# Kernel optimization log

Measured on AMD Instinct MI355X. Metric: run time of the kernel, lower is better.

## Reference

```python
import jax, jax.numpy as jnp
import numpy as np

N_STATE = 1024
N_HEAD = 16
HEAD_DIM = N_STATE // N_HEAD
SCALE = HEAD_DIM ** (-0.25)


def setup_inputs() -> dict:
    key = jax.random.key(0)
    ks = jax.random.split(key, 9)
    B, S, D = 32, 1500, N_STATE
    std = 1.0 / np.sqrt(D)
    return {
        "hidden_states": jax.random.normal(ks[0], (B, 1, D), dtype=jnp.float32),
        "encoder_output": jax.random.normal(ks[1], (B, S, D), dtype=jnp.float32),
        "Wq": jax.random.normal(ks[2], (D, D), dtype=jnp.float32) * std,
        "bq": jax.random.normal(ks[3], (D,), dtype=jnp.float32) * std,
        "Wk": jax.random.normal(ks[4], (D, D), dtype=jnp.float32) * std,
        "Wv": jax.random.normal(ks[5], (D, D), dtype=jnp.float32) * std,
        "bv": jax.random.normal(ks[6], (D,), dtype=jnp.float32) * std,
        "Wo": jax.random.normal(ks[7], (D, D), dtype=jnp.float32) * std,
        "bo": jax.random.normal(ks[8], (D,), dtype=jnp.float32) * std,
    }


def reference(hidden_states, encoder_output, Wq, bq, Wk, Wv, bv, Wo, bo):
    B = hidden_states.shape[0]
    S = encoder_output.shape[1]
    # projections (torch F.linear: x @ W.T + b)
    q = hidden_states @ Wq.T + bq                  # [B, 1, D]
    k_original = encoder_output @ Wk.T             # [B, S, D] (no bias)
    v_original = encoder_output @ Wv.T + bv        # [B, S, D]

    q = q.reshape(B, 1, N_HEAD, HEAD_DIM).transpose(0, 2, 1, 3)         # [B,H,1,hd]
    k = k_original.reshape(B, S, N_HEAD, HEAD_DIM).transpose(0, 2, 1, 3)  # [B,H,S,hd]
    v = v_original.reshape(B, S, N_HEAD, HEAD_DIM).transpose(0, 2, 1, 3)  # [B,H,S,hd]

    # pre-scaled q and k, scores in fp32 softmax then cast back
    attn_weights = jnp.einsum('bhqd,bhkd->bhqk', q * SCALE, k * SCALE)  # [B,H,1,S]
    attn_weights = jax.nn.softmax(attn_weights.astype(jnp.float32), axis=-1).astype(q.dtype)
    attn_output = jnp.einsum('bhqk,bhkd->bhqd', attn_weights, v)        # [B,H,1,hd]
    attn_output = attn_output.transpose(0, 2, 1, 3).reshape(B, 1, N_STATE)
    attn_output = attn_output @ Wo.T + bo
    return attn_output, k_original, v_original
```

## Files before the change

kernel.cpp:

```cpp
#include <hip/hip_runtime.h>
#include <cstdint>
#include <cstddef>

#define D_MODEL 1024
#define NH      16
#define HD      64
#define B_SZ    32
#define SEQ     1500
#define MROWS   (B_SZ * SEQ)
#define KD      1024
#define NCH     16
#define PSTR    68

typedef __attribute__((ext_vector_type(8))) short bf16x8;
typedef __attribute__((ext_vector_type(4))) float f32x4;
typedef unsigned short u16;

__device__ __forceinline__ u16 f2b(float f) {
  unsigned int x = __float_as_uint(f);
  x = (x + 0x7FFFu + ((x >> 16) & 1u)) >> 16;
  return (u16)x;
}

#define CAST_BLOCKS 3072
#define QPROJ_BLOCKS 64

__global__ __launch_bounds__(256) void cast_all_q(const float* __restrict__ enc,
                                                  const float* __restrict__ Wk,
                                                  const float* __restrict__ Wv,
                                                  const float* __restrict__ hs,
                                                  const float* __restrict__ Wq,
                                                  const float* __restrict__ bq,
                                                  u16* __restrict__ encb,
                                                  u16* __restrict__ wkvb,
                                                  float* __restrict__ qs) {
  const int tid = threadIdx.x;
  if (blockIdx.x < CAST_BLOCKS) {
    const int NA = MROWS * KD / 8;
    const int NW = KD * KD / 8;
    int stride = CAST_BLOCKS * 256;
    for (int i = blockIdx.x * 256 + tid; i < NA + 2 * NW; i += stride) {
      const float* s; u16* d;
      if (i < NA)            { s = enc + (size_t)i * 8;            d = encb + (size_t)i * 8; }
      else if (i < NA + NW)  { size_t j = i - NA;      s = Wk + j * 8; d = wkvb + j * 8; }
      else                   { size_t j = i - NA - NW; s = Wv + j * 8; d = wkvb + (size_t)NW * 8 + j * 8; }
      const float4* s4 = reinterpret_cast<const float4*>(s);
      float4 a = s4[0], b = s4[1];
      u16 u[8];
      u[0]=f2b(a.x); u[1]=f2b(a.y); u[2]=f2b(a.z); u[3]=f2b(a.w);
      u[4]=f2b(b.x); u[5]=f2b(b.y); u[6]=f2b(b.z); u[7]=f2b(b.w);
      *reinterpret_cast<uint4*>(d) = *reinterpret_cast<const uint4*>(u);
    }
  } else {
    const int qb = blockIdx.x - CAST_BLOCKS;
    const int n  = qb * 16 + (tid & 15);
    const int bb = tid >> 4;
    const float4* wp  = (const float4*)(Wq + (size_t)n * D_MODEL);
    const float4* x0p = (const float4*)(hs + (size_t)bb * D_MODEL);
    const float4* x1p = (const float4*)(hs + (size_t)(bb + 16) * D_MODEL);
    float a0 = 0.f, a1 = 0.f;
    #pragma unroll 8
    for (int i = 0; i < D_MODEL / 4; ++i) {
      float4 w = wp[i], x0 = x0p[i], x1 = x1p[i];
      a0 += w.x * x0.x + w.y * x0.y + w.z * x0.z + w.w * x0.w;
      a1 += w.x * x1.x + w.y * x1.y + w.z * x1.z + w.w * x1.w;
    }
    const float bqn = bq[n];
    qs[(size_t)bb * D_MODEL + n]        = (a0 + bqn) * 0.125f;
    qs[(size_t)(bb + 16) * D_MODEL + n] = (a1 + bqn) * 0.125f;
  }
}

#define GBM 128
#define GBN 256
#define GBK 32
#define GNT (KD / GBK)

__device__ __forceinline__ void stageA(const u16* __restrict__ Ag, u16* lbuf,
                                       long m0, int kt, int tid) {
  int c = tid;
  int r = c >> 2, cp = c & 3;
  int scp = cp ^ ((r >> 1) & 3);
  const u16* src = Ag + (m0 + r) * (long)KD + kt * GBK + scp * 8;
  __builtin_amdgcn_global_load_lds((const __attribute__((address_space(1))) void*)src,
      (__attribute__((address_space(3))) void*)(lbuf + (size_t)c * 8), 16, 0, 0);
}

__device__ __forceinline__ void stageB(const u16* __restrict__ Bg, u16* lbuf,
                                       int n0, int kt, int tid) {
  #pragma unroll
  for (int L = 0; L < 2; ++L) {
    int c = tid + L * 512;
    int r = c >> 2, cp = c & 3;
    int scp = cp ^ ((r >> 1) & 3);
    const u16* src = Bg + (size_t)(n0 + r) * KD + kt * GBK + scp * 8;
    __builtin_amdgcn_global_load_lds((const __attribute__((address_space(1))) void*)src,
        (__attribute__((address_space(3))) void*)(lbuf + (size_t)c * 8), 16, 0, 0);
  }
}

__device__ __forceinline__ bf16x8 ldFrag(const u16* buf, int row, int lane) {
  int r  = row + (lane & 15);
  int ch = (lane >> 4) ^ ((r >> 1) & 3);
  return *(const bf16x8*)(buf + (size_t)r * GBK + ch * 8);
}

__global__ __launch_bounds__(512, 4) void gemm_kv(const u16* __restrict__ A,
                                                  const u16* __restrict__ Bm,
                                                  const float* __restrict__ bv,
                                                  float* __restrict__ Kout,
                                                  float* __restrict__ Vout) {
  __shared__ __align__(16) char smem[2 * (GBM + GBN) * GBK * 2];
  u16* sA0 = (u16*)smem;
  u16* sA1 = sA0 + GBM * GBK;
  u16* sB0 = sA1 + GBM * GBK;
  u16* sB1 = sB0 + GBN * GBK;

  const int tid  = threadIdx.x;
  const int lane = tid & 63;
  const int wid  = tid >> 6;
  const int wr   = wid >> 2;
  const int wc   = wid & 3;

  int bx = (blockIdx.x & 7) * (gridDim.x >> 3) + (blockIdx.x >> 3);
  const int  mt = bx >> 3;
  const int  nt = bx & 7;
  const long m0 = (long)mt * GBM;
  const int  n0 = nt * GBN;

  stageA(A, sA0, m0, 0, tid);
  stageB(Bm, sB0, n0, 0, tid);
  stageA(A, sA1, m0, 1, tid);
  stageB(Bm, sB1, n0, 1, tid);

  f32x4 acc[4][4] = {};

  for (int t = 0; t < GNT; ++t) {
    if (t == GNT - 1) { asm volatile("s_waitcnt vmcnt(0)" ::: "memory"); }
    else              { asm volatile("s_waitcnt vmcnt(3)" ::: "memory"); }
    __builtin_amdgcn_s_barrier();

    const u16* cA = (t & 1) ? sA1 : sA0;
    const u16* cB = (t & 1) ? sB1 : sB0;
    bf16x8 af[4], bfr[4];
    #pragma unroll
    for (int mf = 0; mf < 4; ++mf) af[mf]  = ldFrag(cA, wr * 64 + mf * 16, lane);
    #pragma unroll
    for (int nf = 0; nf < 4; ++nf) bfr[nf] = ldFrag(cB, wc * 64 + nf * 16, lane);
    asm volatile("s_waitcnt lgkmcnt(0)" ::: "memory");
    __builtin_amdgcn_s_barrier();

    if (t + 2 < GNT) {
      u16* pA = (t & 1) ? sA1 : sA0;
      u16* pB = (t & 1) ? sB1 : sB0;
      stageA(A, pA, m0, t + 2, tid);
      stageB(Bm, pB, n0, t + 2, tid);
    }

    #pragma unroll
    for (int mf = 0; mf < 4; ++mf)
      #pragma unroll
      for (int nf = 0; nf < 4; ++nf)
        acc[mf][nf] = __builtin_amdgcn_mfma_f32_16x16x32_bf16(af[mf], bfr[nf], acc[mf][nf], 0, 0, 0);
  }

  __syncthreads();
  float (*ep)[260] = (float(*)[260])smem;

  const bool isV = (nt >= 4);
  float* Co = isV ? Vout : Kout;
  const int ncol0 = isV ? (n0 - 1024) : n0;
  float4 bias4[4];
  #pragma unroll
  for (int k = 0; k < 4; ++k) {
    int c4 = (tid + 512 * k) & 63;
    bias4[k] = isV ? reinterpret_cast<const float4*>(bv)[(ncol0 >> 2) + c4]
                   : make_float4(0.f, 0.f, 0.f, 0.f);
  }

  #pragma unroll
  for (int p = 0; p < 4; ++p) {
    if (wr == (p >> 1)) {
      const int mfb = (p & 1) * 2;
      #pragma unroll
      for (int mm = 0; mm < 2; ++mm)
        #pragma unroll
        for (int nf = 0; nf < 4; ++nf)
          #pragma unroll
          for (int r = 0; r < 4; ++r)
            ep[mm * 16 + (lane >> 4) * 4 + r][wc * 64 + nf * 16 + (lane & 15)] =
                acc[mfb + mm][nf][r];
    }
    __syncthreads();
    #pragma unroll
    for (int k = 0; k < 4; ++k) {
      int idx = tid + 512 * k;
      int row = idx >> 6;
      int c4  = idx & 63;
      long grow = m0 + p * 32 + row;
      float4 v = *reinterpret_cast<const float4*>(&ep[row][c4 * 4]);
      v.x += bias4[k].x; v.y += bias4[k].y; v.z += bias4[k].z; v.w += bias4[k].w;
      *reinterpret_cast<float4*>(&Co[grow * D_MODEL + ncol0 + c4 * 4]) = v;
    }
    __syncthreads();
  }
}

__global__ __launch_bounds__(256) void attn_part(const float* __restrict__ qs,
                                                 const float* __restrict__ K,
                                                 const float* __restrict__ V,
                                                 float* __restrict__ part) {
  const int blk = blockIdx.x;
  const int bh = blk >> 2, qb = blk & 3;
  const int b = bh >> 4, h = bh & 15;
  const int w = threadIdx.x >> 6;
  const int lane = threadIdx.x & 63;
  const int c = qb * 4 + w;
  const int s0 = (c * SEQ) >> 4;
  const int L = (((c + 1) * SEQ) >> 4) - s0;

  __shared__ float scs[4][96];
  float* sc = scs[w];

  const int j  = lane & 15;
  const int rg = lane >> 4;
  const float4 q4 = *(const float4*)(qs + (size_t)b * D_MODEL + h * HD + j * 4);

  float lmax = -1e30f;
  for (int i = rg; i < L; i += 4) {
    const float4 k4 = *(const float4*)(K + (size_t)(b * SEQ + s0 + i) * D_MODEL + h * HD + j * 4);
    float p = q4.x * k4.x + q4.y * k4.y + q4.z * k4.z + q4.w * k4.w;
    p += __shfl_xor(p, 1);
    p += __shfl_xor(p, 2);
    p += __shfl_xor(p, 4);
    p += __shfl_xor(p, 8);
    if (j == 0) sc[i] = p;
    lmax = fmaxf(lmax, p);
  }
  lmax = fmaxf(lmax, __shfl_xor(lmax, 16));
  lmax = fmaxf(lmax, __shfl_xor(lmax, 32));
  const float m = lmax;
  asm volatile("s_waitcnt lgkmcnt(0)" ::: "memory");

  float lsum = 0.f;
  for (int i = lane; i < L; i += 64) {
    float p = __expf(sc[i] - m);
    sc[i] = p;
    lsum += p;
  }
  lsum += __shfl_xor(lsum, 1);
  lsum += __shfl_xor(lsum, 2);
  lsum += __shfl_xor(lsum, 4);
  lsum += __shfl_xor(lsum, 8);
  lsum += __shfl_xor(lsum, 16);
  lsum += __shfl_xor(lsum, 32);
  asm volatile("s_waitcnt lgkmcnt(0)" ::: "memory");

  float4 a4 = make_float4(0.f, 0.f, 0.f, 0.f);
  for (int i = rg; i < L; i += 4) {
    float p = sc[i];
    float4 v4 = *(const float4*)(V + (size_t)(b * SEQ + s0 + i) * D_MODEL + h * HD + j * 4);
    a4.x += p * v4.x; a4.y += p * v4.y; a4.z += p * v4.z; a4.w += p * v4.w;
  }
  a4.x += __shfl_xor(a4.x, 16); a4.x += __shfl_xor(a4.x, 32);
  a4.y += __shfl_xor(a4.y, 16); a4.y += __shfl_xor(a4.y, 32);
  a4.z += __shfl_xor(a4.z, 16); a4.z += __shfl_xor(a4.z, 32);
  a4.w += __shfl_xor(a4.w, 16); a4.w += __shfl_xor(a4.w, 32);

  float* pp = part + (size_t)(bh * NCH + c) * PSTR;
  if (lane < 16) *(float4*)(pp + lane * 4) = a4;
  if (lane == 0) { pp[64] = m; pp[65] = lsum; }
}

__global__ __launch_bounds__(256) void oproj_comb(const float* __restrict__ part,
                                                  const float* __restrict__ Wo,
                                                  const float* __restrict__ bo,
                                                  float* __restrict__ out) {
  const int b = blockIdx.x >> 3, ch = blockIdx.x & 7;
  const int tid = threadIdx.x;
  __shared__ float xs[D_MODEL];

  {
    const int h = tid >> 4;
    const int d = (tid & 15) * 4;
    const float* pp = part + (size_t)(b * NH + h) * NCH * PSTR;
    float M = -1e30f;
    #pragma unroll
    for (int cc = 0; cc < NCH; ++cc) M = fmaxf(M, pp[cc * PSTR + 64]);
    float Lsum = 0.f;
    float4 o = make_float4(0.f, 0.f, 0.f, 0.f);
    #pragma unroll
    for (int cc = 0; cc < NCH; ++cc) {
      const float wgt = __expf(pp[cc * PSTR + 64] - M);
      Lsum += pp[cc * PSTR + 65] * wgt;
      float4 pv = *(const float4*)(pp + cc * PSTR + d);
      o.x += pv.x * wgt; o.y += pv.y * wgt; o.z += pv.z * wgt; o.w += pv.w * wgt;
    }
    const float inv = 1.0f / Lsum;
    xs[h * HD + d]     = o.x * inv;
    xs[h * HD + d + 1] = o.y * inv;
    xs[h * HD + d + 2] = o.z * inv;
    xs[h * HD + d + 3] = o.w * inv;
  }
  __syncthreads();

  const int n = ch * 128 + (tid >> 1);
  const int half = tid & 1;
  const float4* wp = (const float4*)(Wo + (size_t)n * D_MODEL + half * 512);
  const float4* xp = (const float4*)xs + half * 128;
  float a = 0.f;
  #pragma unroll 8
  for (int i = 0; i < 128; ++i) {
    float4 w = wp[i], xv = xp[i];
    a += w.x * xv.x + w.y * xv.y + w.z * xv.z + w.w * xv.w;
  }
  a += __shfl_xor(a, 1);
  if (!half) out[(size_t)b * D_MODEL + n] = a + bo[n];
}

extern "C" void kernel_launch(void* const* d_in, const int* in_sizes, int n_in,
                              void* d_out, int out_size, void* d_ws, size_t ws_size,
                              hipStream_t stream) {
  const float* hs  = (const float*)d_in[0];
  const float* enc = (const float*)d_in[1];
  const float* Wq  = (const float*)d_in[2];
  const float* bq  = (const float*)d_in[3];
  const float* Wk  = (const float*)d_in[4];
  const float* Wv  = (const float*)d_in[5];
  const float* bv  = (const float*)d_in[6];
  const float* Wo  = (const float*)d_in[7];
  const float* bo  = (const float*)d_in[8];

  float* out   = (float*)d_out;
  float* attnO = out;
  float* Kout  = out + 32768;
  float* Vout  = Kout + (size_t)MROWS * D_MODEL;

  char* ws = (char*)d_ws;
  const size_t off_wkvb = (size_t)MROWS * D_MODEL * 2;
  const size_t off_qs   = off_wkvb + 4194304;
  const size_t off_part = off_qs + 131072;

  u16*   encb = (u16*)ws;
  u16*   wkvb = (u16*)(ws + off_wkvb);
  float* qs   = (float*)(ws + off_qs);
  float* part = (float*)(ws + off_part);

  cast_all_q<<<CAST_BLOCKS + QPROJ_BLOCKS, 256, 0, stream>>>(enc, Wk, Wv, hs, Wq, bq,
                                                             encb, wkvb, qs);

  gemm_kv<<<(MROWS / GBM) * (2048 / GBN), 512, 0, stream>>>(encb, wkvb, bv, Kout, Vout);

  attn_part<<<B_SZ * NH * 4, 256, 0, stream>>>(qs, Kout, Vout, part);
  oproj_comb<<<B_SZ * 8, 256, 0, stream>>>(part, Wo, bo, attnO);
}
```

Before: 458.4 us.

## Restructure attention partials to process all heads per block with online softmax

Each block now handles one batch and one sequence chunk across all 16 heads. Each 16-lane group owns one head, so every K/V row read is a contiguous 4KB row instead of a 256B per-head slice. The three-pass shared-memory softmax is replaced by a single-pass online softmax that rescales the running max, sum and PV accumulator, which removes the LDS traffic and waits. This adds two extra exps per row and leaves each thread with a serial loop of about 94 rows, using fewer blocks (512 instead of 2048).

```diff
diff --git a/kernel.cpp b/kernel.cpp
--- a/kernel.cpp
+++ b/kernel.cpp
@@ -210,66 +210,65 @@
                                                  const float* __restrict__ K,
                                                  const float* __restrict__ V,
                                                  float* __restrict__ part) {
-  const int blk = blockIdx.x;
-  const int bh = blk >> 2, qb = blk & 3;
-  const int b = bh >> 4, h = bh & 15;
-  const int w = threadIdx.x >> 6;
-  const int lane = threadIdx.x & 63;
-  const int c = qb * 4 + w;
+  const int b = blockIdx.x >> 4;
+  const int c = blockIdx.x & 15;
+  const int tid = threadIdx.x;
+  const int h = tid >> 4;
+  const int j = tid & 15;
   const int s0 = (c * SEQ) >> 4;
-  const int L = (((c + 1) * SEQ) >> 4) - s0;
-
-  __shared__ float scs[4][96];
-  float* sc = scs[w];
-
-  const int j  = lane & 15;
-  const int rg = lane >> 4;
-  const float4 q4 = *(const float4*)(qs + (size_t)b * D_MODEL + h * HD + j * 4);
-
-  float lmax = -1e30f;
-  for (int i = rg; i < L; i += 4) {
-    const float4 k4 = *(const float4*)(K + (size_t)(b * SEQ + s0 + i) * D_MODEL + h * HD + j * 4);
-    float p = q4.x * k4.x + q4.y * k4.y + q4.z * k4.z + q4.w * k4.w;
-    p += __shfl_xor(p, 1);
-    p += __shfl_xor(p, 2);
-    p += __shfl_xor(p, 4);
-    p += __shfl_xor(p, 8);
-    if (j == 0) sc[i] = p;
-    lmax = fmaxf(lmax, p);
-  }
-  lmax = fmaxf(lmax, __shfl_xor(lmax, 16));
-  lmax = fmaxf(lmax, __shfl_xor(lmax, 32));
-  const float m = lmax;
-  asm volatile("s_waitcnt lgkmcnt(0)" ::: "memory");
-
-  float lsum = 0.f;
-  for (int i = lane; i < L; i += 64) {
-    float p = __expf(sc[i] - m);
-    sc[i] = p;
-    lsum += p;
-  }
-  lsum += __shfl_xor(lsum, 1);
-  lsum += __shfl_xor(lsum, 2);
-  lsum += __shfl_xor(lsum, 4);
-  lsum += __shfl_xor(lsum, 8);
-  lsum += __shfl_xor(lsum, 16);
-  lsum += __shfl_xor(lsum, 32);
-  asm volatile("s_waitcnt lgkmcnt(0)" ::: "memory");
-
-  float4 a4 = make_float4(0.f, 0.f, 0.f, 0.f);
-  for (int i = rg; i < L; i += 4) {
-    float p = sc[i];
-    float4 v4 = *(const float4*)(V + (size_t)(b * SEQ + s0 + i) * D_MODEL + h * HD + j * 4);
-    a4.x += p * v4.x; a4.y += p * v4.y; a4.z += p * v4.z; a4.w += p * v4.w;
-  }
-  a4.x += __shfl_xor(a4.x, 16); a4.x += __shfl_xor(a4.x, 32);
-  a4.y += __shfl_xor(a4.y, 16); a4.y += __shfl_xor(a4.y, 32);
-  a4.z += __shfl_xor(a4.z, 16); a4.z += __shfl_xor(a4.z, 32);
-  a4.w += __shfl_xor(a4.w, 16); a4.w += __shfl_xor(a4.w, 32);
-
-  float* pp = part + (size_t)(bh * NCH + c) * PSTR;
-  if (lane < 16) *(float4*)(pp + lane * 4) = a4;
-  if (lane == 0) { pp[64] = m; pp[65] = lsum; }
+  const int s1 = (((c + 1) * SEQ) >> 4);
+
+  const float4 q4 = ((const float4*)(qs + (size_t)b * D_MODEL))[tid];
+  float m = -1e30f, l = 0.f;
+  float4 pv = make_float4(0.f, 0.f, 0.f, 0.f);
+
+  int i = s0;
+  for (; i + 2 <= s1; i += 2) {
+    const float4 kA = ((const float4*)(K + (size_t)(b * SEQ + i) * D_MODEL))[tid];
+    const float4 vA = ((const float4*)(V + (size_t)(b * SEQ + i) * D_MODEL))[tid];
+    const float4 kB = ((const float4*)(K + (size_t)(b * SEQ + i + 1) * D_MODEL))[tid];
+    const float4 vB = ((const float4*)(V + (size_t)(b * SEQ + i + 1) * D_MODEL))[tid];
+
+    float sA = kA.x * q4.x + kA.y * q4.y + kA.z * q4.z + kA.w * q4.w;
+    sA += __shfl_xor(sA, 1); sA += __shfl_xor(sA, 2);
+    sA += __shfl_xor(sA, 4); sA += __shfl_xor(sA, 8);
+    float mn = fmaxf(m, sA);
+    float sc = __expf(m - mn);
+    float p  = __expf(sA - mn);
+    m = mn;
+    l = l * sc + p;
+    pv.x = pv.x * sc + p * vA.x; pv.y = pv.y * sc + p * vA.y;
+    pv.z = pv.z * sc + p * vA.z; pv.w = pv.w * sc + p * vA.w;
+
+    float sB = kB.x * q4.x + kB.y * q4.y + kB.z * q4.z + kB.w * q4.w;
+    sB += __shfl_xor(sB, 1); sB += __shfl_xor(sB, 2);
+    sB += __shfl_xor(sB, 4); sB += __shfl_xor(sB, 8);
+    mn = fmaxf(m, sB);
+    sc = __expf(m - mn);
+    p  = __expf(sB - mn);
+    m = mn;
+    l = l * sc + p;
+    pv.x = pv.x * sc + p * vB.x; pv.y = pv.y * sc + p * vB.y;
+    pv.z = pv.z * sc + p * vB.z; pv.w = pv.w * sc + p * vB.w;
+  }
+  if (i < s1) {
+    const float4 kA = ((const float4*)(K + (size_t)(b * SEQ + i) * D_MODEL))[tid];
+    const float4 vA = ((const float4*)(V + (size_t)(b * SEQ + i) * D_MODEL))[tid];
+    float sA = kA.x * q4.x + kA.y * q4.y + kA.z * q4.z + kA.w * q4.w;
+    sA += __shfl_xor(sA, 1); sA += __shfl_xor(sA, 2);
+    sA += __shfl_xor(sA, 4); sA += __shfl_xor(sA, 8);
+    float mn = fmaxf(m, sA);
+    float sc = __expf(m - mn);
+    float p  = __expf(sA - mn);
+    m = mn;
+    l = l * sc + p;
+    pv.x = pv.x * sc + p * vA.x; pv.y = pv.y * sc + p * vA.y;
+    pv.z = pv.z * sc + p * vA.z; pv.w = pv.w * sc + p * vA.w;
+  }
+
+  float* pp = part + ((size_t)(b * NH + h) * NCH + c) * PSTR;
+  *(float4*)(pp + j * 4) = pv;
+  if (j == 0) { pp[64] = m; pp[65] = l; }
 }
 
 __global__ __launch_bounds__(256) void oproj_comb(const float* __restrict__ part,
@@ -351,6 +350,6 @@
 
   gemm_kv<<<(MROWS / GBM) * (2048 / GBN), 512, 0, stream>>>(encb, wkvb, bv, Kout, Vout);
 
-  attn_part<<<B_SZ * NH * 4, 256, 0, stream>>>(qs, Kout, Vout, part);
+  attn_part<<<B_SZ * NCH, 256, 0, stream>>>(qs, Kout, Vout, part);
   oproj_comb<<<B_SZ * 8, 256, 0, stream>>>(part, Wo, bo, attnO);
 }
```

New measurement: 453.6 us. Within noise of the previous version (-1.0%).
